# Kernel optimization log

Hardware: AMD Instinct MI355X
Metric: run time of the kernel (lower is better)

Reference implementation:

```python
import jax, jax.numpy as jnp
from jax import lax
import numpy as np

B, C, T = 16, 512, 4096
COEFF_INIT = 0.04


def setup_inputs() -> dict:
    key = jax.random.key(0)
    k1, k2 = jax.random.split(key)
    x = jax.random.normal(k1, (B, C, T), dtype=jnp.float32)
    # learned per-channel smoothing coefficients, initialized like the module
    weights = jnp.ones((C,), dtype=jnp.float32) * COEFF_INIT
    return {"x": x, "weights": weights}


def reference(x, weights):
    # clamp weights to [0, 1] (mirrors the in-place no-grad clamp; values stay
    # unchanged here since coeff_init is inside the range)
    s = jnp.clip(weights, 0.0, 1.0)  # [C]
    xt = jnp.moveaxis(x, 2, 0)       # [T, B, C]
    init = xt[0]                      # y_0 = x_0

    def step(acc, sample):
        acc = s * sample + (1.0 - s) * acc
        return acc, acc

    _, ys = lax.scan(step, init, xt[1:])          # [T-1, B, C]
    out = jnp.concatenate([init[None], ys], axis=0)  # [T, B, C]
    return jnp.moveaxis(out, 0, 2)                   # [B, C, T]
```

## Files before the change

kernel.cpp:

```cpp
#include <hip/hip_runtime.h>


constexpr int T_LEN = 4096;
constexpr int C_LEN = 512;
constexpr int BLOCK = 256;
constexpr int NCHUNK = 16;

typedef float nfloat4 __attribute__((ext_vector_type(4)));

__global__ __launch_bounds__(BLOCK, 4) void ema_row_kernel(
    const float* __restrict__ x,
    const float* __restrict__ w,
    float* __restrict__ y)
{
    const int lane = threadIdx.x & 63;
    const int wv   = threadIdx.x >> 6;
    const int row  = (blockIdx.x << 2) + wv;
    const int c    = row & (C_LEN - 1);

    float s = w[c];
    s = fminf(fmaxf(s, 0.0f), 1.0f);
    const float a = 1.0f - s;

    const nfloat4* xp = (const nfloat4*)(x + (size_t)row * T_LEN);
    nfloat4*       yp = (nfloat4*)(y + (size_t)row * T_LEN);

    nfloat4 v[NCHUNK];
    #pragma unroll
    for (int m = 0; m < NCHUNK; ++m)
        v[m] = xp[(m << 6) + lane];

    const float a2 = a * a, a3 = a2 * a, a4 = a2 * a2;

    float powl = 1.0f, tq = a4;
    #pragma unroll
    for (int b = 0; b < 6; ++b) {
        if ((lane >> b) & 1) powl *= tq;
        tq *= tq;
    }
    float a256 = a4;
    #pragma unroll
    for (int q = 0; q < 6; ++q) a256 *= a256;

    float E = 0.0f;

    #pragma unroll
    for (int t = 0; t < 4; ++t) {
        float S[4];

        #pragma unroll
        for (int k = 0; k < 4; ++k) {
            const int m = (t << 2) + k;
            float l0 = s * v[m].x;
            if (m == 0 && lane == 0) l0 = v[m].x;
            float l1 = fmaf(a, l0, s * v[m].y);
            float l2 = fmaf(a, l1, s * v[m].z);
            float l3 = fmaf(a, l2, s * v[m].w);
            v[m].x = l0; v[m].y = l1; v[m].z = l2; v[m].w = l3;
            S[k] = l3;
        }

        float wgt = a4;
        #pragma unroll
        for (int d = 1; d < 64; d <<= 1) {
            #pragma unroll
            for (int k = 0; k < 4; ++k) {
                float up = __shfl_up(S[k], d, 64);
                if (lane >= d) S[k] = fmaf(wgt, up, S[k]);
            }
            wgt *= wgt;
        }

        #pragma unroll
        for (int k = 0; k < 4; ++k) {
            const int m = (t << 2) + k;
            float Sx   = __shfl_up(S[k], 1, 64);
            float base = (lane == 0) ? 0.0f : Sx;
            float P    = fmaf(powl, E, base);
            nfloat4 o;
            o.x = fmaf(a,  P, v[m].x);
            o.y = fmaf(a2, P, v[m].y);
            o.z = fmaf(a3, P, v[m].z);
            o.w = fmaf(a4, P, v[m].w);
            __builtin_nontemporal_store(o, &yp[(m << 6) + lane]);

            float Tk = __shfl(S[k], 63, 64);
            E = fmaf(a256, E, Tk);
        }
    }
}

extern "C" void kernel_launch(void* const* d_in, const int* in_sizes, int n_in,
                              void* d_out, int out_size, void* d_ws, size_t ws_size,
                              hipStream_t stream) {
    const float* x = (const float*)d_in[0];
    const float* w = (const float*)d_in[1];
    float* y = (float*)d_out;

    const int rows = out_size / T_LEN;
    ema_row_kernel<<<rows / 4, BLOCK, 0, stream>>>(x, w, y);
}
```

Before: 237.2 us.

## Stream rows through double-buffered tiles with a persistent fixed grid

Instead of loading a whole 4096-element row into registers per wave, each wave now processes two rows in tiles of 1024 elements. The next tile's loads are issued before the current tile is scanned, and the grid is fixed at 1024 blocks. This cuts register pressure so occupancy can rise, and overlaps memory latency with the scan. The grid size is hardcoded to the problem shape, and the a256 factor is now taken from the loop-final wgt value.

```diff
diff --git a/kernel.cpp b/kernel.cpp
--- a/kernel.cpp
+++ b/kernel.cpp
@@ -4,59 +4,70 @@
 constexpr int T_LEN = 4096;
 constexpr int C_LEN = 512;
 constexpr int BLOCK = 256;
-constexpr int NCHUNK = 16;
+constexpr int GRID  = 1024;
+constexpr int RPW   = 2;
+constexpr int NITEM = RPW * 4;
 
-typedef float nfloat4 __attribute__((ext_vector_type(4)));
+typedef float nf4 __attribute__((ext_vector_type(4)));
 
-__global__ __launch_bounds__(BLOCK, 4) void ema_row_kernel(
+__global__ __launch_bounds__(BLOCK) void ema_stream_kernel(
     const float* __restrict__ x,
     const float* __restrict__ w,
     float* __restrict__ y)
 {
     const int lane = threadIdx.x & 63;
-    const int wv   = threadIdx.x >> 6;
-    const int row  = (blockIdx.x << 2) + wv;
-    const int c    = row & (C_LEN - 1);
+    const int wid  = (blockIdx.x << 2) + (threadIdx.x >> 6);
 
-    float s = w[c];
-    s = fminf(fmaxf(s, 0.0f), 1.0f);
-    const float a = 1.0f - s;
+    const size_t rbase = (size_t)wid * RPW * 1024;
+    const nf4* xp = (const nf4*)x;
+    nf4*       yp = (nf4*)y;
 
-    const nfloat4* xp = (const nfloat4*)(x + (size_t)row * T_LEN);
-    nfloat4*       yp = (nfloat4*)(y + (size_t)row * T_LEN);
-
-    nfloat4 v[NCHUNK];
-    #pragma unroll
-    for (int m = 0; m < NCHUNK; ++m)
-        v[m] = xp[(m << 6) + lane];
-
-    const float a2 = a * a, a3 = a2 * a, a4 = a2 * a2;
-
-    float powl = 1.0f, tq = a4;
-    #pragma unroll
-    for (int b = 0; b < 6; ++b) {
-        if ((lane >> b) & 1) powl *= tq;
-        tq *= tq;
-    }
-    float a256 = a4;
-    #pragma unroll
-    for (int q = 0; q < 6; ++q) a256 *= a256;
-
-    float E = 0.0f;
+    nf4 buf[2][4];
 
     #pragma unroll
-    for (int t = 0; t < 4; ++t) {
+    for (int k = 0; k < 4; ++k)
+        buf[0][k] = xp[rbase + (k << 6) + lane];
+
+    float s = 0.f, a = 0.f, a2 = 0.f, a3 = 0.f, a4 = 0.f;
+    float powl = 0.f, E = 0.f;
+
+    #pragma unroll
+    for (int j = 0; j < NITEM; ++j) {
+        const int tile = j & 3;
+
+        if (j + 1 < NITEM) {
+            const size_t nb = rbase + (size_t)(j + 1) * 256;
+            #pragma unroll
+            for (int k = 0; k < 4; ++k)
+                buf[(j + 1) & 1][k] = xp[nb + (k << 6) + lane];
+        }
+
+        if (tile == 0) {
+            const int row = wid * RPW + (j >> 2);
+            const int c   = row & (C_LEN - 1);
+            s  = fminf(fmaxf(w[c], 0.0f), 1.0f);
+            a  = 1.0f - s;
+            a2 = a * a; a3 = a2 * a; a4 = a2 * a2;
+            float tq = a4; powl = 1.0f;
+            #pragma unroll
+            for (int b = 0; b < 6; ++b) {
+                if ((lane >> b) & 1) powl *= tq;
+                tq *= tq;
+            }
+            E = 0.0f;
+        }
+
+        nf4 (&vb)[4] = buf[j & 1];
+
         float S[4];
-
         #pragma unroll
         for (int k = 0; k < 4; ++k) {
-            const int m = (t << 2) + k;
-            float l0 = s * v[m].x;
-            if (m == 0 && lane == 0) l0 = v[m].x;
-            float l1 = fmaf(a, l0, s * v[m].y);
-            float l2 = fmaf(a, l1, s * v[m].z);
-            float l3 = fmaf(a, l2, s * v[m].w);
-            v[m].x = l0; v[m].y = l1; v[m].z = l2; v[m].w = l3;
+            float l0 = s * vb[k].x;
+            if (tile == 0 && k == 0 && lane == 0) l0 = vb[k].x;
+            float l1 = fmaf(a, l0, s * vb[k].y);
+            float l2 = fmaf(a, l1, s * vb[k].z);
+            float l3 = fmaf(a, l2, s * vb[k].w);
+            vb[k].x = l0; vb[k].y = l1; vb[k].z = l2; vb[k].w = l3;
             S[k] = l3;
         }
 
@@ -71,21 +82,21 @@
             wgt *= wgt;
         }
 
+        const size_t ob = rbase + (size_t)j * 256;
         #pragma unroll
         for (int k = 0; k < 4; ++k) {
-            const int m = (t << 2) + k;
             float Sx   = __shfl_up(S[k], 1, 64);
             float base = (lane == 0) ? 0.0f : Sx;
             float P    = fmaf(powl, E, base);
-            nfloat4 o;
-            o.x = fmaf(a,  P, v[m].x);
-            o.y = fmaf(a2, P, v[m].y);
-            o.z = fmaf(a3, P, v[m].z);
-            o.w = fmaf(a4, P, v[m].w);
-            __builtin_nontemporal_store(o, &yp[(m << 6) + lane]);
+            nf4 o;
+            o.x = fmaf(a,  P, vb[k].x);
+            o.y = fmaf(a2, P, vb[k].y);
+            o.z = fmaf(a3, P, vb[k].z);
+            o.w = fmaf(a4, P, vb[k].w);
+            __builtin_nontemporal_store(o, &yp[ob + (k << 6) + lane]);
 
             float Tk = __shfl(S[k], 63, 64);
-            E = fmaf(a256, E, Tk);
+            E = fmaf(wgt, E, Tk);
         }
     }
 }
@@ -97,6 +108,5 @@
     const float* w = (const float*)d_in[1];
     float* y = (float*)d_out;
 
-    const int rows = out_size / T_LEN;
-    ema_row_kernel<<<rows / 4, BLOCK, 0, stream>>>(x, w, y);
+    ema_stream_kernel<<<GRID, BLOCK, 0, stream>>>(x, w, y);
 }
```

Result: no change. 232.6 us (-2.0%).
